# Kernel optimization log

Measured on AMD Instinct MI355X. Metric: run time of the kernel, lower is better.

The kernel has to match this reference:

```python
import jax, jax.numpy as jnp
import numpy as np


def setup_inputs() -> dict:
    key = jax.random.key(0)
    k1, k2 = jax.random.split(key)
    B, S, D = 4, 2048, 1024
    x = jax.random.normal(k1, (B, S, D), dtype=jnp.float32)
    # uniform initializer in keras is small; scale to keep softmax well-behaved
    kernel = jax.random.normal(k2, (3, D, D), dtype=jnp.float32) * 0.02
    return {"x": x, "kernel": kernel}


def reference(x, kernel):
    # x: [B, S, D], kernel: [3, D, D]
    D = x.shape[-1]
    q = jnp.einsum('bsd,de->bse', x, kernel[0])
    k = jnp.einsum('bsd,de->bse', x, kernel[1])
    v = jnp.einsum('bsd,de->bse', x, kernel[2])
    scores = jnp.einsum('bqe,bke->bqk', q, k) / jnp.sqrt(jnp.float32(D))
    attn = jax.nn.softmax(scores, axis=-1)
    return jnp.einsum('bqk,bke->bqe', attn, v)
```

## Files before the change

kernel.cpp:

```cpp
#include <hip/hip_runtime.h>
#include <hip/hip_bf16.h>
#include <cstdint>

typedef __bf16 bf16x8 __attribute__((ext_vector_type(8)));
typedef float f32x4 __attribute__((ext_vector_type(4)));

__device__ __forceinline__ unsigned short f2bf(float f) {
  union { float f; uint32_t u; } a; a.f = f;
  uint32_t r = a.u + 0x7fffu + ((a.u >> 16) & 1u);
  return (unsigned short)(r >> 16);
}
__device__ __forceinline__ float bf2f(unsigned short b) {
  union { uint32_t u; float f; } a; a.u = ((uint32_t)b) << 16;
  return a.f;
}
__device__ __forceinline__ void gload_lds16(const unsigned short* g, unsigned short* l) {
  __builtin_amdgcn_global_load_lds(
      (const __attribute__((address_space(1))) void*)g,
      (__attribute__((address_space(3))) void*)l, 16, 0, 0);
}

__global__ void cast_x_kernel(const float* __restrict__ x, unsigned short* __restrict__ xb) {
  size_t i = ((size_t)blockIdx.x * 256 + threadIdx.x) * 8;
  float4 a = *(const float4*)(x + i);
  float4 b = *(const float4*)(x + i + 4);
  uint4 o;
  o.x = (uint32_t)f2bf(a.x) | ((uint32_t)f2bf(a.y) << 16);
  o.y = (uint32_t)f2bf(a.z) | ((uint32_t)f2bf(a.w) << 16);
  o.z = (uint32_t)f2bf(b.x) | ((uint32_t)f2bf(b.y) << 16);
  o.w = (uint32_t)f2bf(b.z) | ((uint32_t)f2bf(b.w) << 16);
  *(uint4*)(xb + i) = o;
}

__global__ void cast_w_kernel(const float* __restrict__ W, unsigned short* __restrict__ Wt) {
  __shared__ float tile[32][33];
  const int z = blockIdx.z;
  const float* Wz = W + (size_t)z * 1024 * 1024;
  unsigned short* Wtz = Wt + (size_t)z * 1024 * 1024;
  const int x0 = blockIdx.x * 32, y0 = blockIdx.y * 32;
  const int tx = threadIdx.x, ty = threadIdx.y;
#pragma unroll
  for (int i = 0; i < 32; i += 8)
    tile[ty + i][tx] = Wz[(size_t)(y0 + ty + i) * 1024 + x0 + tx];
  __syncthreads();
#pragma unroll
  for (int i = 0; i < 32; i += 8)
    Wtz[(size_t)(x0 + ty + i) * 1024 + y0 + tx] = f2bf(tile[tx][ty + i]);
}

template <int MODE>
__global__ void __launch_bounds__(256)
gemm_bt(const unsigned short* __restrict__ Aall,
        const unsigned short* __restrict__ Btall,
        void* __restrict__ Call,
        int K, int ldc, long sA, long sB, long sC, float scale) {
  __shared__ unsigned short As[128 * 64];
  __shared__ unsigned short Bs[128 * 64];
  const int t = threadIdx.x;
  const int lane = t & 63;
  const int quad = lane >> 4;
  const int l15 = lane & 15;
  const int wave = t >> 6;
  const int wm = (wave >> 1) * 64;
  const int wn = (wave & 1) * 64;
  const int z = blockIdx.z;

  const unsigned short* A = Aall + (size_t)z * sA + (size_t)blockIdx.x * 128 * K;
  const unsigned short* Bt = Btall + (size_t)z * sB + (size_t)blockIdx.y * 128 * K;

  const int srow = t >> 3;
  const int scol = ((t & 7) ^ (srow & 7)) * 8;
  const unsigned short* ga = A + (size_t)srow * K + scol;
  const unsigned short* gb = Bt + (size_t)srow * K + scol;
  unsigned short* lA = As + t * 8;
  unsigned short* lB = Bs + t * 8;

  const int c0 = (quad ^ (l15 & 7)) * 8;
  const unsigned short* aP = As + (size_t)(wm + l15) * 64;
  const unsigned short* bP = Bs + (size_t)(wn + l15) * 64;

  f32x4 acc[4][4];
#pragma unroll
  for (int i = 0; i < 4; i++)
#pragma unroll
    for (int j = 0; j < 4; j++) acc[i][j] = (f32x4){0.f, 0.f, 0.f, 0.f};

  for (int k0 = 0; k0 < K; k0 += 64) {
#pragma unroll
    for (int i = 0; i < 4; i++) {
      gload_lds16(ga + (size_t)i * 32 * K + k0, lA + i * 2048);
      gload_lds16(gb + (size_t)i * 32 * K + k0, lB + i * 2048);
    }
    __syncthreads();
#pragma unroll
    for (int h = 0; h < 2; h++) {
      const int co = c0 ^ (h * 32);
      bf16x8 a[4], b[4];
#pragma unroll
      for (int i = 0; i < 4; i++) a[i] = *(const bf16x8*)(aP + i * 1024 + co);
#pragma unroll
      for (int j = 0; j < 4; j++) b[j] = *(const bf16x8*)(bP + j * 1024 + co);
#pragma unroll
      for (int i = 0; i < 4; i++)
#pragma unroll
        for (int j = 0; j < 4; j++)
          acc[i][j] = __builtin_amdgcn_mfma_f32_16x16x32_bf16(a[i], b[j], acc[i][j], 0, 0, 0);
    }
    __syncthreads();
  }

  const int mbase = blockIdx.x * 128 + wm + quad * 4;
  const int nbase = blockIdx.y * 128 + wn + l15;

  if (MODE == 0) {
    unsigned short* C = (unsigned short*)Call + (size_t)z * sC;
#pragma unroll
    for (int mi = 0; mi < 4; mi++)
#pragma unroll
      for (int ni = 0; ni < 4; ni++) {
        const int m = mbase + mi * 16, n = nbase + ni * 16;
#pragma unroll
        for (int r = 0; r < 4; r++)
          C[(size_t)(m + r) * ldc + n] = f2bf(acc[mi][ni][r] * scale);
      }
  } else if (MODE == 3) {
    float* C = (float*)Call + (size_t)z * sC;
#pragma unroll
    for (int mi = 0; mi < 4; mi++)
#pragma unroll
      for (int ni = 0; ni < 4; ni++) {
        const int m = mbase + mi * 16, n = nbase + ni * 16;
#pragma unroll
        for (int r = 0; r < 4; r++)
          C[(size_t)(m + r) * ldc + n] = acc[mi][ni][r];
      }
  } else {
    unsigned short* C = (unsigned short*)Call;
#pragma unroll
    for (int mi = 0; mi < 4; mi++) {
      const int m = mbase + mi * 16;
      const int b = m >> 11, s = m & 2047;
#pragma unroll
      for (int ni = 0; ni < 4; ni++) {
        const int n = nbase + ni * 16;
        uint2 val;
        val.x = (uint32_t)f2bf(acc[mi][ni][0]) | ((uint32_t)f2bf(acc[mi][ni][1]) << 16);
        val.y = (uint32_t)f2bf(acc[mi][ni][2]) | ((uint32_t)f2bf(acc[mi][ni][3]) << 16);
        *(uint2*)(C + (size_t)b * 2097152 + (size_t)n * 2048 + s) = val;
      }
    }
  }
}

__global__ void softmax_kernel(unsigned short* __restrict__ S) {
  __shared__ float redmax[4];
  __shared__ float redsum[4];
  const size_t row = blockIdx.x;
  unsigned short* p = S + row * 2048;
  const int t = threadIdx.x;
  uint4 raw = *(const uint4*)(p + t * 8);
  const unsigned short* up = (const unsigned short*)&raw;
  float v[8];
#pragma unroll
  for (int i = 0; i < 8; i++) v[i] = bf2f(up[i]);
  float m = v[0];
#pragma unroll
  for (int i = 1; i < 8; i++) m = fmaxf(m, v[i]);
#pragma unroll
  for (int off = 32; off > 0; off >>= 1) m = fmaxf(m, __shfl_xor(m, off));
  if ((t & 63) == 0) redmax[t >> 6] = m;
  __syncthreads();
  m = fmaxf(fmaxf(redmax[0], redmax[1]), fmaxf(redmax[2], redmax[3]));
  float s = 0.f;
#pragma unroll
  for (int i = 0; i < 8; i++) { v[i] = __expf(v[i] - m); s += v[i]; }
#pragma unroll
  for (int off = 32; off > 0; off >>= 1) s += __shfl_xor(s, off);
  if ((t & 63) == 0) redsum[t >> 6] = s;
  __syncthreads();
  s = redsum[0] + redsum[1] + redsum[2] + redsum[3];
  const float inv = 1.f / s;
  uint4 o;
  o.x = (uint32_t)f2bf(v[0] * inv) | ((uint32_t)f2bf(v[1] * inv) << 16);
  o.y = (uint32_t)f2bf(v[2] * inv) | ((uint32_t)f2bf(v[3] * inv) << 16);
  o.z = (uint32_t)f2bf(v[4] * inv) | ((uint32_t)f2bf(v[5] * inv) << 16);
  o.w = (uint32_t)f2bf(v[6] * inv) | ((uint32_t)f2bf(v[7] * inv) << 16);
  *(uint4*)(p + t * 8) = o;
}

extern "C" void kernel_launch(void* const* d_in, const int* in_sizes, int n_in,
                              void* d_out, int out_size, void* d_ws, size_t ws_size,
                              hipStream_t stream) {
  const float* x = (const float*)d_in[0];
  const float* W = (const float*)d_in[1];
  float* out = (float*)d_out;
  char* ws = (char*)d_ws;
  unsigned short* xb = (unsigned short*)(ws);
  unsigned short* Wt = (unsigned short*)(ws + (16ll << 20));
  unsigned short* Q  = (unsigned short*)(ws + (22ll << 20));
  unsigned short* Kb = (unsigned short*)(ws + (38ll << 20));
  unsigned short* Vt = (unsigned short*)(ws + (54ll << 20));
  unsigned short* Sb = (unsigned short*)(ws + (70ll << 20));

  cast_x_kernel<<<4096, 256, 0, stream>>>(x, xb);
  cast_w_kernel<<<dim3(32, 32, 3), dim3(32, 8), 0, stream>>>(W, Wt);

  gemm_bt<0><<<dim3(64, 8, 2), 256, 0, stream>>>(
      xb, Wt, Q, 1024, 1024, 0L, 1048576L, 8388608L, 1.0f);
  gemm_bt<2><<<dim3(64, 8, 1), 256, 0, stream>>>(
      xb, Wt + 2 * 1048576, Vt, 1024, 0, 0L, 0L, 0L, 1.0f);
  gemm_bt<0><<<dim3(16, 16, 4), 256, 0, stream>>>(
      Q, Kb, Sb, 1024, 2048, 2097152L, 2097152L, 4194304L, 0.03125f);
  softmax_kernel<<<8192, 256, 0, stream>>>(Sb);
  gemm_bt<3><<<dim3(16, 8, 4), 256, 0, stream>>>(
      Sb, Vt, out, 2048, 1024, 4194304L, 2097152L, 2097152L, 1.0f);
}
```

Measured before the change: 270.2 us.

## Double-buffer LDS tiles in GEMM and merge Q/K/V projections into one launch

The GEMM main loop now uses two LDS buffers with a K-step of 32. The next tile's global-to-LDS load is issued before computing on the current one, so only one barrier per iteration is needed. The LDS swizzle changes to match the 32-wide rows. The Q, K and V projections are also fused into one launch through a new mode, where z<2 writes Q/K and z=2 writes a transposed V via an extra pointer. This trades a smaller K-step per barrier for more load/compute overlap and one fewer launch.

```diff
diff --git a/kernel.cpp b/kernel.cpp
--- a/kernel.cpp
+++ b/kernel.cpp
@@ -52,10 +52,10 @@
 __global__ void __launch_bounds__(256)
 gemm_bt(const unsigned short* __restrict__ Aall,
         const unsigned short* __restrict__ Btall,
-        void* __restrict__ Call,
+        void* __restrict__ Call, unsigned short* __restrict__ VtPtr,
         int K, int ldc, long sA, long sB, long sC, float scale) {
-  __shared__ unsigned short As[128 * 64];
-  __shared__ unsigned short Bs[128 * 64];
+  __shared__ unsigned short As[2][4096];
+  __shared__ unsigned short Bs[2][4096];
   const int t = threadIdx.x;
   const int lane = t & 63;
   const int quad = lane >> 4;
@@ -68,16 +68,14 @@
   const unsigned short* A = Aall + (size_t)z * sA + (size_t)blockIdx.x * 128 * K;
   const unsigned short* Bt = Btall + (size_t)z * sB + (size_t)blockIdx.y * 128 * K;
 
-  const int srow = t >> 3;
-  const int scol = ((t & 7) ^ (srow & 7)) * 8;
+  const int srow = t >> 2;
+  const int scol = (((t & 3) ^ ((srow >> 1) & 3)) * 8);
   const unsigned short* ga = A + (size_t)srow * K + scol;
   const unsigned short* gb = Bt + (size_t)srow * K + scol;
-  unsigned short* lA = As + t * 8;
-  unsigned short* lB = Bs + t * 8;
-
-  const int c0 = (quad ^ (l15 & 7)) * 8;
-  const unsigned short* aP = As + (size_t)(wm + l15) * 64;
-  const unsigned short* bP = Bs + (size_t)(wn + l15) * 64;
+  const size_t rowskip = (size_t)64 * K;
+
+  const int aOff = (wm + l15) * 32 + (quad ^ ((l15 >> 1) & 3)) * 8;
+  const int bOff = (wn + l15) * 32 + (quad ^ ((l15 >> 1) & 3)) * 8;
 
   f32x4 acc[4][4];
 #pragma unroll
@@ -85,34 +83,39 @@
 #pragma unroll
     for (int j = 0; j < 4; j++) acc[i][j] = (f32x4){0.f, 0.f, 0.f, 0.f};
 
-  for (int k0 = 0; k0 < K; k0 += 64) {
-#pragma unroll
-    for (int i = 0; i < 4; i++) {
-      gload_lds16(ga + (size_t)i * 32 * K + k0, lA + i * 2048);
-      gload_lds16(gb + (size_t)i * 32 * K + k0, lB + i * 2048);
+  gload_lds16(ga, &As[0][t * 8]);
+  gload_lds16(ga + rowskip, &As[0][2048 + t * 8]);
+  gload_lds16(gb, &Bs[0][t * 8]);
+  gload_lds16(gb + rowskip, &Bs[0][2048 + t * 8]);
+
+  int buf = 0;
+  for (int k0 = 0; k0 < K; k0 += 32, buf ^= 1) {
+    __syncthreads();
+    if (k0 + 32 < K) {
+      const int kn = k0 + 32;
+      gload_lds16(ga + kn, &As[buf ^ 1][t * 8]);
+      gload_lds16(ga + rowskip + kn, &As[buf ^ 1][2048 + t * 8]);
+      gload_lds16(gb + kn, &Bs[buf ^ 1][t * 8]);
+      gload_lds16(gb + rowskip + kn, &Bs[buf ^ 1][2048 + t * 8]);
     }
-    __syncthreads();
-#pragma unroll
-    for (int h = 0; h < 2; h++) {
-      const int co = c0 ^ (h * 32);
-      bf16x8 a[4], b[4];
-#pragma unroll
-      for (int i = 0; i < 4; i++) a[i] = *(const bf16x8*)(aP + i * 1024 + co);
-#pragma unroll
-      for (int j = 0; j < 4; j++) b[j] = *(const bf16x8*)(bP + j * 1024 + co);
-#pragma unroll
-      for (int i = 0; i < 4; i++)
-#pragma unroll
-        for (int j = 0; j < 4; j++)
-          acc[i][j] = __builtin_amdgcn_mfma_f32_16x16x32_bf16(a[i], b[j], acc[i][j], 0, 0, 0);
-    }
-    __syncthreads();
+    const unsigned short* aB = &As[buf][aOff];
+    const unsigned short* bB = &Bs[buf][bOff];
+    bf16x8 a[4], b[4];
+#pragma unroll
+    for (int i = 0; i < 4; i++) a[i] = *(const bf16x8*)(aB + i * 512);
+#pragma unroll
+    for (int j = 0; j < 4; j++) b[j] = *(const bf16x8*)(bB + j * 512);
+#pragma unroll
+    for (int i = 0; i < 4; i++)
+#pragma unroll
+      for (int j = 0; j < 4; j++)
+        acc[i][j] = __builtin_amdgcn_mfma_f32_16x16x32_bf16(a[i], b[j], acc[i][j], 0, 0, 0);
   }
 
   const int mbase = blockIdx.x * 128 + wm + quad * 4;
   const int nbase = blockIdx.y * 128 + wn + l15;
 
-  if (MODE == 0) {
+  if (MODE == 0 || (MODE == 4 && z < 2)) {
     unsigned short* C = (unsigned short*)Call + (size_t)z * sC;
 #pragma unroll
     for (int mi = 0; mi < 4; mi++)
@@ -135,7 +138,7 @@
           C[(size_t)(m + r) * ldc + n] = acc[mi][ni][r];
       }
   } else {
-    unsigned short* C = (unsigned short*)Call;
+    unsigned short* C = VtPtr;
 #pragma unroll
     for (int mi = 0; mi < 4; mi++) {
       const int m = mbase + mi * 16;
@@ -205,13 +208,11 @@
   cast_x_kernel<<<4096, 256, 0, stream>>>(x, xb);
   cast_w_kernel<<<dim3(32, 32, 3), dim3(32, 8), 0, stream>>>(W, Wt);
 
-  gemm_bt<0><<<dim3(64, 8, 2), 256, 0, stream>>>(
-      xb, Wt, Q, 1024, 1024, 0L, 1048576L, 8388608L, 1.0f);
-  gemm_bt<2><<<dim3(64, 8, 1), 256, 0, stream>>>(
-      xb, Wt + 2 * 1048576, Vt, 1024, 0, 0L, 0L, 0L, 1.0f);
+  gemm_bt<4><<<dim3(64, 8, 3), 256, 0, stream>>>(
+      xb, Wt, Q, Vt, 1024, 1024, 0L, 1048576L, 8388608L, 1.0f);
   gemm_bt<0><<<dim3(16, 16, 4), 256, 0, stream>>>(
-      Q, Kb, Sb, 1024, 2048, 2097152L, 2097152L, 4194304L, 0.03125f);
+      Q, Kb, Sb, nullptr, 1024, 2048, 2097152L, 2097152L, 4194304L, 0.03125f);
   softmax_kernel<<<8192, 256, 0, stream>>>(Sb);
   gemm_bt<3><<<dim3(16, 8, 4), 256, 0, stream>>>(
-      Sb, Vt, out, 2048, 1024, 4194304L, 2097152L, 2097152L, 1.0f);
-}
+      Sb, Vt, out, nullptr, 2048, 1024, 4194304L, 2097152L, 2097152L, 1.0f);
+}
```

Result: no change. 270.4 us (+0.1%).
